# Kernel optimization log

Measured on AMD Instinct MI355X. Metric: run time of the kernel, lower is better.

Reference implementation:

```python
import jax, jax.numpy as jnp
import numpy as np

N_QUBITS = 4
N_LAYERS = 3
BATCH = 1000000


def _apply_1q(state, m00, m01, m10, m11, q):
    # state: [B, 2,2,2,2]; apply 2x2 gate on qubit axis q (broadcastable m's)
    s = jnp.moveaxis(state, q + 1, 1)
    a0, a1 = s[:, 0], s[:, 1]
    out = jnp.stack([m00 * a0 + m01 * a1, m10 * a0 + m11 * a1], axis=1)
    return jnp.moveaxis(out, 1, q + 1)


def _rx(state, theta, q):
    # PennyLane RX: [[cos(t/2), -i sin(t/2)], [-i sin(t/2), cos(t/2)]]; theta is per-batch [B]
    h = theta * 0.5
    sh = (-1,) + (1,) * (N_QUBITS - 1)  # broadcast over remaining qubit axes
    c = jnp.cos(h).reshape(sh)
    s = jnp.sin(h).reshape(sh)
    return _apply_1q(state, c, -1j * s, -1j * s, c, q)


def _ry(state, theta, q):
    # PennyLane RY: [[cos, -sin], [sin, cos]] of t/2; theta is a shared scalar
    h = theta * 0.5
    c = jnp.cos(h)
    s = jnp.sin(h)
    return _apply_1q(state, c, -s, s, c, q)


def _cnot(state, ctrl, tgt):
    # ctrl < tgt in the ladder; flip target amplitudes where control bit == 1
    s = jnp.moveaxis(state, ctrl + 1, 1)
    s = jnp.moveaxis(s, tgt + 1, 2)
    s = jnp.concatenate([s[:, :1], s[:, 1:, ::-1]], axis=1)
    s = jnp.moveaxis(s, 2, tgt + 1)
    return jnp.moveaxis(s, 1, ctrl + 1)


def _expval_z(probs, w):
    pm = jnp.moveaxis(probs, w + 1, 1)
    pm = pm.reshape(pm.shape[0], 2, -1)
    return pm[:, 0].sum(-1) - pm[:, 1].sum(-1)


def _circuit(angles, weights):
    # angles: [B, n_qubits]; weights: [n_layers, n_qubits]
    B = angles.shape[0]
    state = jnp.zeros((B,) + (2,) * N_QUBITS, jnp.complex64)
    state = state.at[(slice(None),) + (0,) * N_QUBITS].set(1.0)
    for layer in range(N_LAYERS):
        for i in range(N_QUBITS):
            state = _rx(state, angles[:, i], i)
        for i in range(N_QUBITS):
            state = _ry(state, weights[layer, i], i)
        for i in range(N_QUBITS - 1):
            state = _cnot(state, i, i + 1)
    probs = jnp.real(state * jnp.conj(state))
    return jnp.stack([_expval_z(probs, 0), _expval_z(probs, 1)], axis=-1)  # [B, 2]


def setup_inputs() -> dict:
    key = jax.random.key(0)
    k1, k2 = jax.random.split(key)
    x = jax.random.normal(k1, (BATCH, N_QUBITS), dtype=jnp.float32)
    weights = jax.random.uniform(k2, (N_LAYERS, N_QUBITS), dtype=jnp.float32,
                                 minval=0.0, maxval=2.0 * np.pi)
    w_input = jnp.ones((N_QUBITS,), jnp.float32)
    w_output = jnp.full((2,), 50.0, jnp.float32)
    return {"x": x, "w_input": w_input, "weights": weights, "w_output": w_output}


def reference(x, w_input, weights, w_output):
    angles = jnp.arctan(x * w_input)          # input scaling + atan embedding
    out = _circuit(angles, weights)           # [B, 2] PauliZ expvals in [-1, 1]
    return (1.0 + out) / 2.0 * w_output       # rescale to [0, w_output]
```

## Files before the change

### kernel.cpp

```cpp
#include <hip/hip_runtime.h>


__device__ __forceinline__ void apply_rx(float (&re)[16], float (&im)[16],
                                         float c, float s, const int st) {
#pragma unroll
    for (int i = 0; i < 16; ++i) {
        if (i & st) continue;
        const int j = i | st;
        float a0r = re[i], a0i = im[i], a1r = re[j], a1i = im[j];
        re[i] = c * a0r + s * a1i;
        im[i] = c * a0i - s * a1r;
        re[j] = c * a1r + s * a0i;
        im[j] = c * a1i - s * a0r;
    }
}

__device__ __forceinline__ void apply_ry(float (&re)[16], float (&im)[16],
                                         float c, float s, const int st) {
#pragma unroll
    for (int i = 0; i < 16; ++i) {
        if (i & st) continue;
        const int j = i | st;
        float a0r = re[i], a0i = im[i], a1r = re[j], a1i = im[j];
        re[i] = c * a0r - s * a1r;
        im[i] = c * a0i - s * a1i;
        re[j] = s * a0r + c * a1r;
        im[j] = s * a0i + c * a1i;
    }
}

__device__ __forceinline__ void apply_cnot(float (&re)[16], float (&im)[16],
                                           const int cm, const int tm) {
#pragma unroll
    for (int i = 0; i < 16; ++i) {
        if ((i & cm) && !(i & tm)) {
            const int j = i | tm;
            float t;
            t = re[i]; re[i] = re[j]; re[j] = t;
            t = im[i]; im[i] = im[j]; im[j] = t;
        }
    }
}

__global__ __launch_bounds__(256) void heaq_kernel(
    const float4* __restrict__ x4,
    const float*  __restrict__ w_input,
    const float*  __restrict__ weights,
    const float*  __restrict__ w_output,
    float2*       __restrict__ out2,
    int B)
{
    int b = blockIdx.x * 256 + threadIdx.x;
    if (b >= B) return;

    float4 xv = x4[b];
    float xs[4] = {xv.x, xv.y, xv.z, xv.w};
    float cx[4], sxv[4];
#pragma unroll
    for (int q = 0; q < 4; ++q) {
        float u = xs[q] * w_input[q];
        float r = __builtin_amdgcn_rsqf(__builtin_fmaf(u, u, 1.0f));
        float c = __builtin_amdgcn_sqrtf(__builtin_fmaf(0.5f, r, 0.5f));
        cx[q] = c;
        sxv[q] = 0.5f * u * r * __builtin_amdgcn_rcpf(c);
    }

    const float K = 0.07957747154594767f;
    float cy[12], sy[12];
#pragma unroll
    for (int t = 0; t < 12; ++t) {
        float rev = __builtin_amdgcn_fractf(weights[t] * K);
        cy[t] = __builtin_amdgcn_cosf(rev);
        sy[t] = __builtin_amdgcn_sinf(rev);
    }

    float vr[4][2], vi[4][2];
#pragma unroll
    for (int q = 0; q < 4; ++q) {
        vr[q][0] = cy[q] * cx[q];
        vi[q][0] = sy[q] * sxv[q];
        vr[q][1] = sy[q] * cx[q];
        vi[q][1] = -cy[q] * sxv[q];
    }
    float p2r[4], p2i[4];
#pragma unroll
    for (int i = 0; i < 4; ++i) {
        const int a = i >> 1, c = i & 1;
        p2r[i] = vr[0][a] * vr[1][c] - vi[0][a] * vi[1][c];
        p2i[i] = vr[0][a] * vi[1][c] + vi[0][a] * vr[1][c];
    }
    float p3r[8], p3i[8];
#pragma unroll
    for (int i = 0; i < 8; ++i) {
        const int h = i >> 1, c = i & 1;
        p3r[i] = p2r[h] * vr[2][c] - p2i[h] * vi[2][c];
        p3i[i] = p2r[h] * vi[2][c] + p2i[h] * vr[2][c];
    }
    float re[16], im[16];
#pragma unroll
    for (int i = 0; i < 16; ++i) {
        const int h = i >> 1, c = i & 1;
        re[i] = p3r[h] * vr[3][c] - p3i[h] * vi[3][c];
        im[i] = p3r[h] * vi[3][c] + p3i[h] * vr[3][c];
    }
    apply_cnot(re, im, 8, 4);
    apply_cnot(re, im, 4, 2);
    apply_cnot(re, im, 2, 1);

    apply_rx(re, im, cx[0], sxv[0], 8);
    apply_rx(re, im, cx[1], sxv[1], 4);
    apply_rx(re, im, cx[2], sxv[2], 2);
    apply_ry(re, im, cy[4], sy[4], 8);
    apply_ry(re, im, cy[5], sy[5], 4);
    apply_ry(re, im, cy[6], sy[6], 2);
    apply_cnot(re, im, 8, 4);
    apply_cnot(re, im, 4, 2);

    apply_rx(re, im, cx[0], sxv[0], 8);
    apply_rx(re, im, cx[1], sxv[1], 4);
    apply_ry(re, im, cy[8], sy[8], 8);
    apply_ry(re, im, cy[9], sy[9], 4);

    float z0 = 0.0f, z1 = 0.0f;
#pragma unroll
    for (int i = 0; i < 16; ++i) {
        float p = re[i] * re[i] + im[i] * im[i];
        z0 += (i & 8) ? -p : p;
        z1 += (((i >> 3) ^ (i >> 2)) & 1) ? -p : p;
    }
    float w0 = w_output[0], w1 = w_output[1];
    out2[b] = make_float2(0.5f * w0 * (1.0f + z0), 0.5f * w1 * (1.0f + z1));
}

extern "C" void kernel_launch(void* const* d_in, const int* in_sizes, int n_in,
                              void* d_out, int out_size, void* d_ws, size_t ws_size,
                              hipStream_t stream) {
    const float* x        = (const float*)d_in[0];
    const float* w_input  = (const float*)d_in[1];
    const float* weights  = (const float*)d_in[2];
    const float* w_output = (const float*)d_in[3];
    float* out = (float*)d_out;

    const int B = in_sizes[0] / 4;

    heaq_kernel<<<(B + 255) / 256, 256, 0, stream>>>(
        (const float4*)x, w_input, weights, w_output, (float2*)out, B);
}
```

Before: 86.57 us.

## Run gate simulation in packed half2 arithmetic with permuted layout and wave-shared trig

Moves the 16-amplitude state into 8 packed half2 registers, so each RX/RY gate runs as packed FP16 FMAs. The first CNOT ladder is folded into a fixed permutation applied when the product state is built, and the later CNOTs become register swaps. The 12 weight sin/cos values are now computed once per lane and broadcast with readlane, replacing 24 transcendentals per thread. This trades fp16 accuracy in the output (scaled by 50) for fewer ALU instructions, though the kernel may already be memory bound.

```diff
diff --git a/kernel.cpp b/kernel.cpp
--- a/kernel.cpp
+++ b/kernel.cpp
@@ -1,45 +1,46 @@
 #include <hip/hip_runtime.h>
+#include <hip/hip_fp16.h>
 
 
-__device__ __forceinline__ void apply_rx(float (&re)[16], float (&im)[16],
-                                         float c, float s, const int st) {
+__device__ __forceinline__ float rdlane(float x, int l) {
+    return __int_as_float(__builtin_amdgcn_readlane(__float_as_int(x), l));
+}
+__device__ __forceinline__ __half2 dup2(float f) {
+    return __half2half2(__float2half(f));
+}
+
+__device__ __forceinline__ void rx2(__half2 (&re2)[8], __half2 (&im2)[8],
+                                    __half2 c, __half2 s, const int m) {
+    __half2 ns = __hneg2(s);
 #pragma unroll
-    for (int i = 0; i < 16; ++i) {
-        if (i & st) continue;
-        const int j = i | st;
-        float a0r = re[i], a0i = im[i], a1r = re[j], a1i = im[j];
-        re[i] = c * a0r + s * a1i;
-        im[i] = c * a0i - s * a1r;
-        re[j] = c * a1r + s * a0i;
-        im[j] = c * a1i - s * a0r;
+    for (int k = 0; k < 8; ++k) {
+        if (k & m) continue;
+        const int k1 = k | m;
+        __half2 r0 = re2[k], i0 = im2[k], r1 = re2[k1], i1 = im2[k1];
+        re2[k]  = __hfma2(c, r0, __hmul2(s,  i1));
+        im2[k]  = __hfma2(c, i0, __hmul2(ns, r1));
+        re2[k1] = __hfma2(c, r1, __hmul2(s,  i0));
+        im2[k1] = __hfma2(c, i1, __hmul2(ns, r0));
     }
 }
 
-__device__ __forceinline__ void apply_ry(float (&re)[16], float (&im)[16],
-                                         float c, float s, const int st) {
+__device__ __forceinline__ void ry2(__half2 (&re2)[8], __half2 (&im2)[8],
+                                    __half2 c, __half2 s, const int m) {
+    __half2 ns = __hneg2(s);
 #pragma unroll
-    for (int i = 0; i < 16; ++i) {
-        if (i & st) continue;
-        const int j = i | st;
-        float a0r = re[i], a0i = im[i], a1r = re[j], a1i = im[j];
-        re[i] = c * a0r - s * a1r;
-        im[i] = c * a0i - s * a1i;
-        re[j] = s * a0r + c * a1r;
-        im[j] = s * a0i + c * a1i;
+    for (int k = 0; k < 8; ++k) {
+        if (k & m) continue;
+        const int k1 = k | m;
+        __half2 r0 = re2[k], i0 = im2[k], r1 = re2[k1], i1 = im2[k1];
+        re2[k]  = __hfma2(c, r0, __hmul2(ns, r1));
+        im2[k]  = __hfma2(c, i0, __hmul2(ns, i1));
+        re2[k1] = __hfma2(s, r0, __hmul2(c, r1));
+        im2[k1] = __hfma2(s, i0, __hmul2(c, i1));
     }
 }
 
-__device__ __forceinline__ void apply_cnot(float (&re)[16], float (&im)[16],
-                                           const int cm, const int tm) {
-#pragma unroll
-    for (int i = 0; i < 16; ++i) {
-        if ((i & cm) && !(i & tm)) {
-            const int j = i | tm;
-            float t;
-            t = re[i]; re[i] = re[j]; re[j] = t;
-            t = im[i]; im[i] = im[j]; im[j] = t;
-        }
-    }
+__device__ __forceinline__ void swap2(__half2 (&a)[8], int x, int y) {
+    __half2 t = a[x]; a[x] = a[y]; a[y] = t;
 }
 
 __global__ __launch_bounds__(256) void heaq_kernel(
@@ -50,37 +51,51 @@
     float2*       __restrict__ out2,
     int B)
 {
-    int b = blockIdx.x * 256 + threadIdx.x;
+    const int lane = threadIdx.x & 63;
+
+    const float K = 0.07957747154594767f;
+    float wv  = weights[lane < 12 ? lane : 0];
+    float rev = __builtin_amdgcn_fractf(wv * K);
+    float sn  = __builtin_amdgcn_sinf(rev);
+    float cn  = __builtin_amdgcn_cosf(rev);
+
+    float cy0 = rdlane(cn, 0), sy0 = rdlane(sn, 0);
+    float cy1 = rdlane(cn, 1), sy1 = rdlane(sn, 1);
+    float cy2 = rdlane(cn, 2), sy2 = rdlane(sn, 2);
+    float cy3 = rdlane(cn, 3), sy3 = rdlane(sn, 3);
+    __half2 cy4h = dup2(rdlane(cn, 4)), sy4h = dup2(rdlane(sn, 4));
+    __half2 cy5h = dup2(rdlane(cn, 5)), sy5h = dup2(rdlane(sn, 5));
+    __half2 cy6h = dup2(rdlane(cn, 6)), sy6h = dup2(rdlane(sn, 6));
+    __half2 cy8h = dup2(rdlane(cn, 8)), sy8h = dup2(rdlane(sn, 8));
+    __half2 cy9h = dup2(rdlane(cn, 9)), sy9h = dup2(rdlane(sn, 9));
+
+    const int b = blockIdx.x * 256 + threadIdx.x;
     if (b >= B) return;
 
     float4 xv = x4[b];
     float xs[4] = {xv.x, xv.y, xv.z, xv.w};
-    float cx[4], sxv[4];
+    float cx[4], sx[4];
 #pragma unroll
     for (int q = 0; q < 4; ++q) {
         float u = xs[q] * w_input[q];
         float r = __builtin_amdgcn_rsqf(__builtin_fmaf(u, u, 1.0f));
         float c = __builtin_amdgcn_sqrtf(__builtin_fmaf(0.5f, r, 0.5f));
         cx[q] = c;
-        sxv[q] = 0.5f * u * r * __builtin_amdgcn_rcpf(c);
+        sx[q] = 0.5f * u * r * __builtin_amdgcn_rcpf(c);
     }
+    __half2 cxh[3], sxh[3];
+#pragma unroll
+    for (int q = 0; q < 3; ++q) { cxh[q] = dup2(cx[q]); sxh[q] = dup2(sx[q]); }
 
-    const float K = 0.07957747154594767f;
-    float cy[12], sy[12];
-#pragma unroll
-    for (int t = 0; t < 12; ++t) {
-        float rev = __builtin_amdgcn_fractf(weights[t] * K);
-        cy[t] = __builtin_amdgcn_cosf(rev);
-        sy[t] = __builtin_amdgcn_sinf(rev);
-    }
-
+    float cys[4] = {cy0, cy1, cy2, cy3};
+    float sys[4] = {sy0, sy1, sy2, sy3};
     float vr[4][2], vi[4][2];
 #pragma unroll
     for (int q = 0; q < 4; ++q) {
-        vr[q][0] = cy[q] * cx[q];
-        vi[q][0] = sy[q] * sxv[q];
-        vr[q][1] = sy[q] * cx[q];
-        vi[q][1] = -cy[q] * sxv[q];
+        vr[q][0] = cys[q] * cx[q];
+        vi[q][0] = sys[q] * sx[q];
+        vr[q][1] = sys[q] * cx[q];
+        vi[q][1] = -cys[q] * sx[q];
     }
     float p2r[4], p2i[4];
 #pragma unroll
@@ -96,37 +111,50 @@
         p3r[i] = p2r[h] * vr[2][c] - p2i[h] * vi[2][c];
         p3i[i] = p2r[h] * vi[2][c] + p2i[h] * vr[2][c];
     }
-    float re[16], im[16];
+
+    constexpr int T[8]  = {0, 1, 3, 2, 7, 6, 4, 5};
+    constexpr int SW[8] = {0, 1, 1, 0, 1, 0, 0, 1};
+    __half2 re2[8], im2[8];
 #pragma unroll
-    for (int i = 0; i < 16; ++i) {
-        const int h = i >> 1, c = i & 1;
-        re[i] = p3r[h] * vr[3][c] - p3i[h] * vi[3][c];
-        im[i] = p3r[h] * vi[3][c] + p3i[h] * vr[3][c];
+    for (int h = 0; h < 8; ++h) {
+        float a0r = p3r[h] * vr[3][0] - p3i[h] * vi[3][0];
+        float a0i = p3r[h] * vi[3][0] + p3i[h] * vr[3][0];
+        float a1r = p3r[h] * vr[3][1] - p3i[h] * vi[3][1];
+        float a1i = p3r[h] * vi[3][1] + p3i[h] * vr[3][1];
+        const int t = T[h];
+        if (SW[h]) {
+            re2[t] = __floats2half2_rn(a1r, a0r);
+            im2[t] = __floats2half2_rn(a1i, a0i);
+        } else {
+            re2[t] = __floats2half2_rn(a0r, a1r);
+            im2[t] = __floats2half2_rn(a0i, a1i);
+        }
     }
-    apply_cnot(re, im, 8, 4);
-    apply_cnot(re, im, 4, 2);
-    apply_cnot(re, im, 2, 1);
 
-    apply_rx(re, im, cx[0], sxv[0], 8);
-    apply_rx(re, im, cx[1], sxv[1], 4);
-    apply_rx(re, im, cx[2], sxv[2], 2);
-    apply_ry(re, im, cy[4], sy[4], 8);
-    apply_ry(re, im, cy[5], sy[5], 4);
-    apply_ry(re, im, cy[6], sy[6], 2);
-    apply_cnot(re, im, 8, 4);
-    apply_cnot(re, im, 4, 2);
+    rx2(re2, im2, cxh[0], sxh[0], 4);
+    rx2(re2, im2, cxh[1], sxh[1], 2);
+    rx2(re2, im2, cxh[2], sxh[2], 1);
+    ry2(re2, im2, cy4h, sy4h, 4);
+    ry2(re2, im2, cy5h, sy5h, 2);
+    ry2(re2, im2, cy6h, sy6h, 1);
+    swap2(re2, 4, 6); swap2(im2, 4, 6);
+    swap2(re2, 5, 7); swap2(im2, 5, 7);
+    swap2(re2, 2, 3); swap2(im2, 2, 3);
+    swap2(re2, 6, 7); swap2(im2, 6, 7);
 
-    apply_rx(re, im, cx[0], sxv[0], 8);
-    apply_rx(re, im, cx[1], sxv[1], 4);
-    apply_ry(re, im, cy[8], sy[8], 8);
-    apply_ry(re, im, cy[9], sy[9], 4);
+    rx2(re2, im2, cxh[0], sxh[0], 4);
+    rx2(re2, im2, cxh[1], sxh[1], 2);
+    ry2(re2, im2, cy8h, sy8h, 4);
+    ry2(re2, im2, cy9h, sy9h, 2);
 
     float z0 = 0.0f, z1 = 0.0f;
 #pragma unroll
-    for (int i = 0; i < 16; ++i) {
-        float p = re[i] * re[i] + im[i] * im[i];
-        z0 += (i & 8) ? -p : p;
-        z1 += (((i >> 3) ^ (i >> 2)) & 1) ? -p : p;
+    for (int k = 0; k < 8; ++k) {
+        __half2 p = __hfma2(re2[k], re2[k], __hmul2(im2[k], im2[k]));
+        float2 pf = __half22float2(p);
+        float ps = pf.x + pf.y;
+        if (k & 4) z0 -= ps; else z0 += ps;
+        if (((k >> 2) ^ (k >> 1)) & 1) z1 -= ps; else z1 += ps;
     }
     float w0 = w_output[0], w1 = w_output[1];
     out2[b] = make_float2(0.5f * w0 * (1.0f + z0), 0.5f * w1 * (1.0f + z1));
```

Result: faster. 84.71 us (-2.1%).
